# Performance work log

Hardware: AMD Instinct MI355X
Metric: run time of the kernel (lower is better)

The kernel has to match this reference:

```python
import jax, jax.numpy as jnp
import numpy as np
from jax import lax

# Hyperparameters from init_kwargs (inference/testing path of the RPN)
PRE_NMS = 6000        # pre_nms_top_n['testing']
POST_NMS = 1000       # post_nms_top_n['testing']
NMS_THRESH = 0.7
MIN_SIZE = 1.0
WX = WY = WW = WH = 1.0                      # reg_weights
BBOX_XFORM_CLIP = float(np.log(1000.0 / 16.0))  # standard BoxCoder clamp on dw/dh


def _decode(deltas, anchors):
    # deltas, anchors: [K, 4] -> decoded boxes [K, 4] (x1,y1,x2,y2)
    wa = anchors[:, 2] - anchors[:, 0]
    ha = anchors[:, 3] - anchors[:, 1]
    cxa = anchors[:, 0] + 0.5 * wa
    cya = anchors[:, 1] + 0.5 * ha
    dx = deltas[:, 0] / WX
    dy = deltas[:, 1] / WY
    dw = jnp.minimum(deltas[:, 2] / WW, BBOX_XFORM_CLIP)
    dh = jnp.minimum(deltas[:, 3] / WH, BBOX_XFORM_CLIP)
    cx = dx * wa + cxa
    cy = dy * ha + cya
    w = jnp.exp(dw) * wa
    h = jnp.exp(dh) * ha
    return jnp.stack([cx - 0.5 * w, cy - 0.5 * h, cx + 0.5 * w, cy + 0.5 * h], axis=-1)


def _nms_keep(boxes, valid, thresh):
    # Sequential NMS over score-sorted boxes [K,4]; 'valid' marks non-removed boxes.
    K = boxes.shape[0]
    x1, y1, x2, y2 = boxes[:, 0], boxes[:, 1], boxes[:, 2], boxes[:, 3]
    areas = (x2 - x1) * (y2 - y1)
    idxs = jnp.arange(K)

    def body(i, keep):
        xx1 = jnp.maximum(x1[i], x1)
        yy1 = jnp.maximum(y1[i], y1)
        xx2 = jnp.minimum(x2[i], x2)
        yy2 = jnp.minimum(y2[i], y2)
        inter = jnp.maximum(xx2 - xx1, 0.0) * jnp.maximum(yy2 - yy1, 0.0)
        iou = inter / (areas[i] + areas - inter + 1e-9)
        suppress = (iou > thresh) & (idxs > i)
        return jnp.where(keep[i], keep & ~suppress, keep)

    return lax.fori_loop(0, K, body, valid)


def _proposals_one(anchors, objectness, deltas, img_h, img_w):
    # anchors [N,4], objectness [N], deltas [N,4] -> proposals [POST_NMS, 4]
    k = min(objectness.shape[0], PRE_NMS)
    scores, idx = lax.top_k(objectness, k)          # topk filter (sorted desc)
    boxes = _decode(deltas[idx], anchors[idx])      # anchor decode on top-k only
    # process_box: clip to image, filter small boxes (masked, not removed, for jit)
    x1 = jnp.clip(boxes[:, 0], 0.0, img_w)
    y1 = jnp.clip(boxes[:, 1], 0.0, img_h)
    x2 = jnp.clip(boxes[:, 2], 0.0, img_w)
    y2 = jnp.clip(boxes[:, 3], 0.0, img_h)
    boxes = jnp.stack([x1, y1, x2, y2], axis=-1)
    valid = ((x2 - x1) >= MIN_SIZE) & ((y2 - y1) >= MIN_SIZE)
    keep = _nms_keep(boxes, valid, NMS_THRESH)
    # Compact kept boxes (score order) into a fixed [POST_NMS,4] buffer, zero-padded
    rank = jnp.cumsum(keep.astype(jnp.int32)) - 1
    tgt = jnp.where(keep & (rank < POST_NMS), rank, POST_NMS)  # POST_NMS -> dropped
    out = jnp.zeros((POST_NMS, 4), boxes.dtype).at[tgt].set(boxes, mode='drop')
    return out


def setup_inputs() -> dict:
    key = jax.random.key(0)
    k1, k2, k3, k4 = jax.random.split(key, 4)
    B, N = 8, 500000
    IMG = 1024
    # Valid anchor boxes: random centers in-image, sizes in [16, 256]
    cxy = jax.random.uniform(k1, (B, N, 2), jnp.float32, 0.0, float(IMG))
    wh = jax.random.uniform(k2, (B, N, 2), jnp.float32, 16.0, 256.0)
    anchors = jnp.concatenate([cxy - 0.5 * wh, cxy + 0.5 * wh], axis=-1)
    objectness = jax.random.normal(k3, (B, N), jnp.float32)
    pred_bbox_delta = 0.1 * jax.random.normal(k4, (B, N, 4), jnp.float32)
    return {"anchors": anchors, "objectness": objectness,
            "pred_bbox_delta": pred_bbox_delta, "img_h": IMG, "img_w": IMG}


def reference(anchors, objectness, pred_bbox_delta, img_h, img_w):
    h, w = float(img_h), float(img_w)
    f = jax.vmap(lambda a, o, d: _proposals_one(a, o, d, h, w))
    return f(anchors, objectness, pred_bbox_delta)  # [B, POST_NMS, 4]
```

## Files before the change

### kernel.cpp

```cpp
#include <hip/hip_runtime.h>
#include <cstdint>
#include <cmath>

#define NBATCH   8
#define NPB      500000
#define PRE_NMS  6000
#define POST_NMS 1000
#define NWORDS   94
#define NBINS    16384
#define CANDCAP  8192
#define BBOX_CLIP 4.135166556742356f
#define NMS_THR  0.7f
#define TI 8
#define TJ 512
#define WIN 16
#define CNT_PAD 64

#define F_SORT 1u
#define F_COMP 2u
#define F_OOB  4u

__device__ __forceinline__ unsigned monot(float f) {
    unsigned b = __float_as_uint(f);
    return (b & 0x80000000u) ? ~b : (b | 0x80000000u);
}

__global__ __launch_bounds__(256) void hist_kernel(const float* __restrict__ obj,
                                                   unsigned* __restrict__ hist) {
    __shared__ unsigned lh[NBINS];
    const int b = blockIdx.y;
    for (int q = threadIdx.x; q < NBINS; q += 256) lh[q] = 0;
    __syncthreads();
    const float* p = obj + (size_t)b * NPB;
    const int stride = gridDim.x * 256;
    for (int i = blockIdx.x * 256 + threadIdx.x; i < NPB; i += stride) {
        unsigned u = monot(p[i]);
        atomicAdd(&lh[u >> 18], 1u);
    }
    __syncthreads();
    unsigned* gh = hist + (size_t)b * NBINS;
    for (int q = threadIdx.x; q < NBINS; q += 256) {
        unsigned v = lh[q];
        if (v) atomicAdd(&gh[q], v);
    }
}

__global__ __launch_bounds__(256) void thresh_kernel(const unsigned* __restrict__ hist,
                                                     unsigned* __restrict__ tbin) {
    __shared__ unsigned part[256], pre[256];
    const int b = blockIdx.x;
    const unsigned* gh = hist + (size_t)b * NBINS;
    const int t = threadIdx.x;
    const int PER = NBINS / 256;
    unsigned s = 0;
    for (int d = 0; d < PER; ++d) s += gh[NBINS - 1 - (t * PER + d)];
    part[t] = s;
    __syncthreads();
    if (t == 0) {
        unsigned run = 0;
        for (int q = 0; q < 256; ++q) { pre[q] = run; run += part[q]; }
    }
    __syncthreads();
    unsigned c = pre[t];
    if (c < PRE_NMS && c + part[t] >= PRE_NMS) {
        unsigned run = c;
        for (int d = 0; d < PER; ++d) {
            int bin = NBINS - 1 - (t * PER + d);
            run += gh[bin];
            if (run >= PRE_NMS) { tbin[b] = (unsigned)bin; break; }
        }
    }
}

__global__ __launch_bounds__(256) void compact_kernel(const float* __restrict__ obj,
                                                      const unsigned* __restrict__ tbin,
                                                      unsigned long long* __restrict__ cand,
                                                      unsigned* __restrict__ ccnt) {
    const int b = blockIdx.y;
    const unsigned T = tbin[b];
    const float* p = obj + (size_t)b * NPB;
    unsigned long long* cb = cand + (size_t)b * CANDCAP;
    const int lane = threadIdx.x & 63;
    const int stride = gridDim.x * 256;
    for (int i = blockIdx.x * 256 + threadIdx.x; i < NPB; i += stride) {
        unsigned u = monot(p[i]);
        const bool pred = (u >> 18) >= T;
        unsigned long long bal = __ballot(pred);
        if (bal == 0) continue;
        unsigned base = 0;
        if (lane == 0) base = atomicAdd(&ccnt[(size_t)b * CNT_PAD], __popcll(bal));
        base = (unsigned)__shfl((int)base, 0);
        if (pred) {
            unsigned pos = base + (unsigned)__popcll(bal & ((1ULL << lane) - 1ULL));
            if (pos < CANDCAP)
                cb[pos] = ((unsigned long long)u << 32) | (unsigned)(~i);
        }
    }
}

__global__ __launch_bounds__(1024) void sort_kernel(const unsigned long long* __restrict__ cand,
                                                    const float* __restrict__ obj,
                                                    unsigned* __restrict__ topk,
                                                    unsigned* __restrict__ flags) {
    __shared__ unsigned long long s[CANDCAP];
    const int b = blockIdx.x, t = threadIdx.x;
    const unsigned long long* cb = cand + (size_t)b * CANDCAP;
    for (int i = t; i < CANDCAP; i += 1024) s[i] = cb[i];
    __syncthreads();
    for (unsigned k = 2; k <= CANDCAP; k <<= 1) {
        for (unsigned j = k >> 1; j > 0; j >>= 1) {
            for (unsigned ii = t; ii < CANDCAP; ii += 1024) {
                unsigned l = ii ^ j;
                if (l > ii) {
                    unsigned long long a = s[ii], c = s[l];
                    bool up = (ii & k) == 0;
                    if (up ? (a < c) : (a > c)) { s[ii] = c; s[l] = a; }
                }
            }
            __syncthreads();
        }
    }
    unsigned f = 0;
    for (int r = t; r < PRE_NMS; r += 1024) {
        unsigned long long c = s[r];
        unsigned idx = ~(unsigned)(c & 0xffffffffULL);
        if (idx >= NPB) { f |= F_OOB; idx = 0; }
        else if (monot(obj[(size_t)b * NPB + idx]) != (unsigned)(c >> 32)) f |= F_COMP;
        if (r < PRE_NMS - 1 && !(c > s[r + 1])) f |= F_SORT;
        topk[(size_t)b * PRE_NMS + r] = idx;
    }
    if (f) atomicOr(&flags[b], f);
}

__global__ __launch_bounds__(256) void decode_kernel(const float* __restrict__ anchors,
                                                     const float* __restrict__ deltas,
                                                     const unsigned* __restrict__ topk,
                                                     const int* __restrict__ imh,
                                                     const int* __restrict__ imw,
                                                     float* __restrict__ boxes,
                                                     float* __restrict__ areas,
                                                     unsigned long long* __restrict__ validm) {
    const int b = blockIdx.y;
    const int r = blockIdx.x * 256 + threadIdx.x;
    const bool active = r < PRE_NMS;
    int vh = imh[0], vw = imw[0];
    float ih = (vh > 0 && vh < (1 << 20)) ? (float)vh : __int_as_float(vh);
    float iw = (vw > 0 && vw < (1 << 20)) ? (float)vw : __int_as_float(vw);
    bool valid = false;
    if (active) {
        unsigned idx = topk[(size_t)b * PRE_NMS + r];
        if (idx >= NPB) idx = 0;
        const float4 a = ((const float4*)anchors)[(size_t)b * NPB + idx];
        const float4 d = ((const float4*)deltas)[(size_t)b * NPB + idx];
        float wa = a.z - a.x, ha = a.w - a.y;
        float cxa = a.x + 0.5f * wa, cya = a.y + 0.5f * ha;
        float dw = fminf(d.z, BBOX_CLIP), dh = fminf(d.w, BBOX_CLIP);
        float cx = __fadd_rn(__fmul_rn(d.x, wa), cxa);
        float cy = __fadd_rn(__fmul_rn(d.y, ha), cya);
        float ew = (float)::exp((double)dw), eh = (float)::exp((double)dh);
        float w = __fmul_rn(ew, wa), h = __fmul_rn(eh, ha);
        float x1 = cx - 0.5f * w, y1 = cy - 0.5f * h;
        float x2 = cx + 0.5f * w, y2 = cy + 0.5f * h;
        x1 = fminf(fmaxf(x1, 0.f), iw); y1 = fminf(fmaxf(y1, 0.f), ih);
        x2 = fminf(fmaxf(x2, 0.f), iw); y2 = fminf(fmaxf(y2, 0.f), ih);
        valid = (x2 - x1 >= 1.0f) && (y2 - y1 >= 1.0f);
        ((float4*)boxes)[(size_t)b * PRE_NMS + r] = make_float4(x1, y1, x2, y2);
        areas[(size_t)b * PRE_NMS + r] = __fmul_rn(x2 - x1, y2 - y1);
    }
    unsigned long long bal = __ballot(valid);
    int w = r >> 6;
    if ((threadIdx.x & 63) == 0 && w < NWORDS) validm[(size_t)b * NWORDS + w] = bal;
}

__global__ __launch_bounds__(256) void mask_kernel(const float* __restrict__ boxes,
                                                   const float* __restrict__ areas,
                                                   unsigned long long* __restrict__ mask) {
    __shared__ float4 sb[TJ];
    __shared__ float  sa[TJ];
    const int b = blockIdx.x & 7;
    const int i0 = (blockIdx.x >> 3) * TI;
    const int jbase = (i0 >> 6) << 6;
    const int wv = threadIdx.x >> 6, ln = threadIdx.x & 63;
    const int ia = i0 + 2 * wv, ic = ia + 1;
    const float4 bA = ((const float4*)boxes)[(size_t)b * PRE_NMS + ia];
    const float4 bC = ((const float4*)boxes)[(size_t)b * PRE_NMS + ic];
    const float aA = areas[(size_t)b * PRE_NMS + ia];
    const float aC = areas[(size_t)b * PRE_NMS + ic];
    unsigned long long* rowA = mask + ((size_t)b * PRE_NMS + ia) * NWORDS;
    unsigned long long* rowC = mask + ((size_t)b * PRE_NMS + ic) * NWORDS;
    const int wA = ia >> 6, wC = ic >> 6;
    for (int t0 = jbase; t0 < NWORDS * 64; t0 += TJ) {
        for (int e = threadIdx.x; e < TJ; e += 256) {
            int j = t0 + e;
            if (j < PRE_NMS) {
                sb[e] = ((const float4*)boxes)[(size_t)b * PRE_NMS + j];
                sa[e] = areas[(size_t)b * PRE_NMS + j];
            } else { sb[e] = make_float4(0.f, 0.f, 0.f, 0.f); sa[e] = 0.f; }
        }
        __syncthreads();
        for (int wl = 0; wl < TJ / 64; ++wl) {
            const int w = (t0 >> 6) + wl;
            if (w >= NWORDS) break;
            const int e = wl * 64 + ln;
            const int j = t0 + e;
            const float4 bj = sb[e];
            const float aj = sa[e];
            bool pA = false, pC = false;
            if (j < PRE_NMS) {
                float xx1 = fmaxf(bA.x, bj.x), yy1 = fmaxf(bA.y, bj.y);
                float xx2 = fminf(bA.z, bj.z), yy2 = fminf(bA.w, bj.w);
                float inter = __fmul_rn(fmaxf(__fsub_rn(xx2, xx1), 0.f),
                                        fmaxf(__fsub_rn(yy2, yy1), 0.f));
                float den = __fadd_rn(__fsub_rn(__fadd_rn(aA, aj), inter), 1e-9f);
                pA = (j > ia) && (__fdiv_rn(inter, den) > NMS_THR);
                xx1 = fmaxf(bC.x, bj.x); yy1 = fmaxf(bC.y, bj.y);
                xx2 = fminf(bC.z, bj.z); yy2 = fminf(bC.w, bj.w);
                inter = __fmul_rn(fmaxf(__fsub_rn(xx2, xx1), 0.f),
                                  fmaxf(__fsub_rn(yy2, yy1), 0.f));
                den = __fadd_rn(__fsub_rn(__fadd_rn(aC, aj), inter), 1e-9f);
                pC = (j > ic) && (__fdiv_rn(inter, den) > NMS_THR);
            }
            unsigned long long mA = __ballot(pA), mC = __ballot(pC);
            if (ln == 0) {
                if (w >= wA) rowA[w] = mA;
                if (w >= wC) rowC[w] = mC;
            }
        }
        __syncthreads();
    }
}

__global__ __launch_bounds__(64) void scan_kernel(const unsigned long long* __restrict__ mask,
                                                  const unsigned long long* __restrict__ validm,
                                                  const float* __restrict__ boxes,
                                                  const unsigned* __restrict__ flags,
                                                  const unsigned* __restrict__ ccnt,
                                                  float* __restrict__ out) {
    const int b = blockIdx.x, lane = threadIdx.x;
    const unsigned long long* mb = mask + (size_t)b * PRE_NMS * NWORDS;
    const int w0 = 2 * lane, w1 = 2 * lane + 1;
    unsigned long long r_lo = (w0 < NWORDS) ? ~validm[(size_t)b * NWORDS + w0] : ~0ULL;
    unsigned long long r_hi = (w1 < NWORDS) ? ~validm[(size_t)b * NWORDS + w1] : ~0ULL;
    int count = 0;

    uint4 MA[WIN], MB[WIN], MC[WIN];
    unsigned long long WA[WIN], WB[WIN], WC[WIN];
    float4 bxA, bxB, bxC;

#define ISSUE(M, W, BX, base_)                                                   \
    {                                                                            \
        const int bb_ = (base_);                                                 \
        const char* rb_ = (const char*)(mb + (size_t)bb_ * NWORDS);              \
        const int wI_ = bb_ >> 6;                                                \
        _Pragma("unroll")                                                        \
        for (int q = 0; q < WIN; ++q) {                                          \
            const char* rp_ = rb_ + (size_t)q * (NWORDS * 8);                    \
            M[q] = *(const uint4*)(rp_ + (size_t)lane * 16);                     \
            W[q] = *(const unsigned long long*)(rp_ + (size_t)wI_ * 8);          \
        }                                                                        \
        BX = (lane < WIN)                                                        \
                 ? ((const float4*)boxes)[(size_t)b * PRE_NMS + bb_ + lane]      \
                 : make_float4(0.f, 0.f, 0.f, 0.f);                              \
    }

#define RESOLVE(M, W, BX, base_)                                                 \
    {                                                                            \
        const int bb_ = (base_);                                                 \
        const int wR_ = bb_ >> 6, s0_ = bb_ & 63;                                \
        const unsigned long long sel_ = (wR_ & 1) ? r_hi : r_lo;                 \
        const int srcl_ = wR_ >> 1;                                              \
        const unsigned lo_ = (unsigned)__shfl((int)(unsigned)(sel_ & 0xffffffffULL), srcl_); \
        const unsigned hi_ = (unsigned)__shfl((int)(unsigned)(sel_ >> 32), srcl_);           \
        const unsigned long long ww_ = ((unsigned long long)hi_ << 32) | lo_;    \
        unsigned cand_ = (unsigned)((~ww_) >> s0_) & 0xFFFFu;                    \
        unsigned kept_ = 0;                                                      \
        const int cb_ = count;                                                   \
        _Pragma("unroll")                                                        \
        for (int q = 0; q < WIN; ++q) {                                          \
            if (((cand_ >> q) & 1u) && count < POST_NMS) {                       \
                kept_ |= 1u << q; ++count;                                       \
                cand_ &= ~(unsigned)(W[q] >> s0_);                               \
            }                                                                    \
        }                                                                        \
        const bool v0_ = (w0 >= wR_), v1_ = (w1 >= wR_);                         \
        _Pragma("unroll")                                                        \
        for (int q = 0; q < WIN; ++q) {                                          \
            if (kept_ & (1u << q)) {                                             \
                const uint4 m_ = M[q];                                           \
                if (v0_) r_lo |= ((unsigned long long)m_.y << 32) | m_.x;        \
                if (v1_) r_hi |= ((unsigned long long)m_.w << 32) | m_.z;        \
            }                                                                    \
        }                                                                        \
        if (lane < WIN && (kept_ & (1u << lane))) {                              \
            const int rank_ = cb_ + __popc(kept_ & ((1u << lane) - 1u));         \
            ((float4*)out)[(size_t)b * POST_NMS + rank_] = BX;                   \
        }                                                                        \
    }

    ISSUE(MA, WA, bxA, 0)
    ISSUE(MB, WB, bxB, WIN)
    bool done = false;
    for (int base = 0; base < PRE_NMS && !done; base += 3 * WIN) {
        const int n2 = base + 2 * WIN;
        ISSUE(MC, WC, bxC, (n2 < PRE_NMS) ? n2 : 0)
        RESOLVE(MA, WA, bxA, base)
        done = (count >= POST_NMS);
        if (!done) {
            const int n3 = base + 3 * WIN;
            ISSUE(MA, WA, bxA, (n3 < PRE_NMS) ? n3 : 0)
            RESOLVE(MB, WB, bxB, base + WIN)
            done = (count >= POST_NMS);
        }
        if (!done) {
            const int n4 = base + 4 * WIN;
            ISSUE(MB, WB, bxB, (n4 < PRE_NMS) ? n4 : 0)
            RESOLVE(MC, WC, bxC, base + 2 * WIN)
            done = (count >= POST_NMS);
        }
    }
#undef ISSUE
#undef RESOLVE

    if (lane == 0) {
        float canary = 0.f;
        const unsigned cc = ccnt[(size_t)b * CNT_PAD];
        const unsigned fl = flags[b];
        if (cc > CANDCAP)       canary = 111000.f;
        else if (cc < PRE_NMS)  canary = 222000.f;
        if (fl & F_SORT)        canary = 333000.f;
        if (fl & F_COMP)        canary = 444000.f;
        if (fl & F_OOB)         canary = 777000.f;
        if (canary != 0.f) out[(size_t)b * POST_NMS * 4] = canary;
    }
}

extern "C" void kernel_launch(void* const* d_in, const int* in_sizes, int n_in,
                              void* d_out, int out_size, void* d_ws, size_t ws_size,
                              hipStream_t stream) {
    const float* anchors = (const float*)d_in[0];
    const float* obj     = (const float*)d_in[1];
    const float* deltas  = (const float*)d_in[2];
    const int*   imh     = (const int*)d_in[3];
    const int*   imw     = (const int*)d_in[4];
    float* out = (float*)d_out;
    char* ws = (char*)d_ws;

    size_t off = 0;
    auto alloc = [&](size_t bytes) {
        size_t o = off;
        off = (off + bytes + 511) & ~(size_t)511;
        return o;
    };
    const size_t HIST  = alloc((size_t)NBATCH * NBINS * 4);
    const size_t TBIN  = alloc((size_t)NBATCH * 4);
    const size_t CCNT  = alloc((size_t)NBATCH * CNT_PAD * 4);
    const size_t FLAGS = alloc((size_t)NBATCH * 4);
    const size_t CAND  = alloc((size_t)NBATCH * CANDCAP * 8);
    const size_t ZEND  = off;
    const size_t TOPK  = alloc((size_t)NBATCH * PRE_NMS * 4);
    const size_t BOX   = alloc((size_t)NBATCH * PRE_NMS * 16);
    const size_t AREA  = alloc((size_t)NBATCH * PRE_NMS * 4);
    const size_t VALID = alloc((size_t)NBATCH * NWORDS * 8);
    const size_t MASK  = alloc((size_t)NBATCH * PRE_NMS * NWORDS * 8);
    (void)alloc(1024);
    if (ws_size < off) return;

    unsigned*            hist   = (unsigned*)(ws + HIST);
    unsigned*            tbin   = (unsigned*)(ws + TBIN);
    unsigned*            ccnt   = (unsigned*)(ws + CCNT);
    unsigned*            flags  = (unsigned*)(ws + FLAGS);
    unsigned long long*  cand   = (unsigned long long*)(ws + CAND);
    unsigned*            topk   = (unsigned*)(ws + TOPK);
    float*               boxes  = (float*)(ws + BOX);
    float*               areas  = (float*)(ws + AREA);
    unsigned long long*  validm = (unsigned long long*)(ws + VALID);
    unsigned long long*  maskp  = (unsigned long long*)(ws + MASK);

    hipMemsetAsync(ws, 0, ZEND, stream);
    hipMemsetAsync(out, 0, (size_t)out_size * sizeof(float), stream);

    hist_kernel   <<<dim3(32, NBATCH), 256, 0, stream>>>(obj, hist);
    thresh_kernel <<<dim3(NBATCH), 256, 0, stream>>>(hist, tbin);
    compact_kernel<<<dim3(128, NBATCH), 256, 0, stream>>>(obj, tbin, cand, ccnt);
    sort_kernel   <<<dim3(NBATCH), 1024, 0, stream>>>(cand, obj, topk, flags);
    decode_kernel <<<dim3((PRE_NMS + 255) / 256, NBATCH), 256, 0, stream>>>(
        anchors, deltas, topk, imh, imw, boxes, areas, validm);
    mask_kernel   <<<dim3((PRE_NMS / TI) * NBATCH), 256, 0, stream>>>(boxes, areas, maskp);
    scan_kernel   <<<dim3(NBATCH), 64, 0, stream>>>(maskp, validm, boxes, flags, ccnt, out);
    (void)in_sizes; (void)n_in; (void)ws_size;
}
```

Measured before the change: 449.0 us.

## Split bitonic sort into parallel chunk sorts plus per-batch merge

New measurement: 405.9 us. 1.11x faster.

```diff
diff --git a/kernel.cpp b/kernel.cpp
--- a/kernel.cpp
+++ b/kernel.cpp
@@ -15,6 +15,7 @@
 #define TJ 512
 #define WIN 16
 #define CNT_PAD 64
+#define SORT_CHUNK 2048
 
 #define F_SORT 1u
 #define F_COMP 2u
@@ -98,16 +99,42 @@
     }
 }
 
-__global__ __launch_bounds__(1024) void sort_kernel(const unsigned long long* __restrict__ cand,
-                                                    const float* __restrict__ obj,
-                                                    unsigned* __restrict__ topk,
-                                                    unsigned* __restrict__ flags) {
+__global__ __launch_bounds__(512) void sort_local_kernel(unsigned long long* __restrict__ cand) {
+    __shared__ unsigned long long s[SORT_CHUNK];
+    const int blk = blockIdx.x;
+    const int b = blk >> 2, c = blk & 3;
+    unsigned long long* cb = cand + (size_t)b * CANDCAP + (size_t)c * SORT_CHUNK;
+    const int t = threadIdx.x;
+    for (int i = t; i < SORT_CHUNK; i += 512) s[i] = cb[i];
+    __syncthreads();
+    for (unsigned k = 2; k <= SORT_CHUNK; k <<= 1) {
+        const bool kfull = (k == SORT_CHUNK);
+        const bool upfull = (c & 1) == 0;
+        for (unsigned j = k >> 1; j > 0; j >>= 1) {
+            for (unsigned ii = t; ii < SORT_CHUNK; ii += 512) {
+                unsigned l = ii ^ j;
+                if (l > ii) {
+                    unsigned long long a = s[ii], d = s[l];
+                    bool up = kfull ? upfull : ((ii & k) == 0);
+                    if (up ? (a < d) : (a > d)) { s[ii] = d; s[l] = a; }
+                }
+            }
+            __syncthreads();
+        }
+    }
+    for (int i = t; i < SORT_CHUNK; i += 512) cb[i] = s[i];
+}
+
+__global__ __launch_bounds__(1024) void sort_merge_kernel(const unsigned long long* __restrict__ cand,
+                                                          const float* __restrict__ obj,
+                                                          unsigned* __restrict__ topk,
+                                                          unsigned* __restrict__ flags) {
     __shared__ unsigned long long s[CANDCAP];
     const int b = blockIdx.x, t = threadIdx.x;
     const unsigned long long* cb = cand + (size_t)b * CANDCAP;
     for (int i = t; i < CANDCAP; i += 1024) s[i] = cb[i];
     __syncthreads();
-    for (unsigned k = 2; k <= CANDCAP; k <<= 1) {
+    for (unsigned k = 2 * SORT_CHUNK; k <= CANDCAP; k <<= 1) {
         for (unsigned j = k >> 1; j > 0; j >>= 1) {
             for (unsigned ii = t; ii < CANDCAP; ii += 1024) {
                 unsigned l = ii ^ j;
@@ -379,13 +406,14 @@
     hipMemsetAsync(ws, 0, ZEND, stream);
     hipMemsetAsync(out, 0, (size_t)out_size * sizeof(float), stream);
 
-    hist_kernel   <<<dim3(32, NBATCH), 256, 0, stream>>>(obj, hist);
-    thresh_kernel <<<dim3(NBATCH), 256, 0, stream>>>(hist, tbin);
-    compact_kernel<<<dim3(128, NBATCH), 256, 0, stream>>>(obj, tbin, cand, ccnt);
-    sort_kernel   <<<dim3(NBATCH), 1024, 0, stream>>>(cand, obj, topk, flags);
-    decode_kernel <<<dim3((PRE_NMS + 255) / 256, NBATCH), 256, 0, stream>>>(
+    hist_kernel      <<<dim3(32, NBATCH), 256, 0, stream>>>(obj, hist);
+    thresh_kernel    <<<dim3(NBATCH), 256, 0, stream>>>(hist, tbin);
+    compact_kernel   <<<dim3(128, NBATCH), 256, 0, stream>>>(obj, tbin, cand, ccnt);
+    sort_local_kernel<<<dim3(NBATCH * (CANDCAP / SORT_CHUNK)), 512, 0, stream>>>(cand);
+    sort_merge_kernel<<<dim3(NBATCH), 1024, 0, stream>>>(cand, obj, topk, flags);
+    decode_kernel    <<<dim3((PRE_NMS + 255) / 256, NBATCH), 256, 0, stream>>>(
         anchors, deltas, topk, imh, imw, boxes, areas, validm);
-    mask_kernel   <<<dim3((PRE_NMS / TI) * NBATCH), 256, 0, stream>>>(boxes, areas, maskp);
-    scan_kernel   <<<dim3(NBATCH), 64, 0, stream>>>(maskp, validm, boxes, flags, ccnt, out);
+    mask_kernel      <<<dim3((PRE_NMS / TI) * NBATCH), 256, 0, stream>>>(boxes, areas, maskp);
+    scan_kernel      <<<dim3(NBATCH), 64, 0, stream>>>(maskp, validm, boxes, flags, ccnt, out);
     (void)in_sizes; (void)n_in; (void)ws_size;
 }
```
